# Kernel optimization log

Hardware: AMD Instinct MI355X
Metric: run time of the kernel (lower is better)

Reference implementation:

```python
import jax, jax.numpy as jnp
import numpy as np

N_NODES = 100000
N_EDGES = 1600000
F_IN = 128
HIDDEN = [128, 128]
F_OUT = 64


def _glorot(key, shape):
    fan_in, fan_out = shape[1], shape[0]
    lim = jnp.sqrt(6.0 / (fan_in + fan_out))
    return jax.random.uniform(key, shape, jnp.float32, -lim, lim)


def setup_inputs() -> dict:
    key = jax.random.key(0)
    ks = jax.random.split(key, 12)
    x = jax.random.normal(ks[0], (N_NODES, F_IN), jnp.float32)
    edge_index = jax.random.randint(ks[1], (2, N_EDGES), 0, N_NODES, jnp.int64)
    dims = [F_IN] + HIDDEN + [F_OUT]  # [128, 128, 128, 64]
    inp = {"x": x, "edge_index": edge_index}
    for i in range(3):
        din, dout = dims[i], dims[i + 1]
        inp[f"Wl{i}"] = _glorot(ks[2 + 3 * i], (dout, din))  # neighbor lin (lin_l)
        inp[f"Wr{i}"] = _glorot(ks[3 + 3 * i], (dout, din))  # root lin (lin_r)
        inp[f"b{i}"] = jnp.zeros((dout,), jnp.float32)
    return inp


def sage_conv(x, src, dst, Wl, Wr, b):
    # PyG SAGEConv, aggr='mean': out = lin_l(mean_{j in N(i)} x_j) + lin_r(x_i) + bias
    msg = x[src]  # [E, Fin] gather from source nodes
    agg = jax.ops.segment_sum(msg, dst, num_segments=N_NODES)  # [N, Fin]
    deg = jax.ops.segment_sum(jnp.ones((src.shape[0],), x.dtype), dst,
                              num_segments=N_NODES)  # [N]
    mean = agg / jnp.maximum(deg, 1.0)[:, None]
    return mean @ Wl.T + x @ Wr.T + b


def reference(x, edge_index, Wl0, Wr0, b0, Wl1, Wr1, b1, Wl2, Wr2, b2):
    src, dst = edge_index[0], edge_index[1]
    h = jax.nn.relu(sage_conv(x, src, dst, Wl0, Wr0, b0))
    h = jax.nn.relu(sage_conv(h, src, dst, Wl1, Wr1, b1))
    out = sage_conv(h, src, dst, Wl2, Wr2, b2)  # final_conv: no relu
    return out
```

## Files before the change

### kernel.cpp

```cpp
#include <hip/hip_runtime.h>

#define NF 128
#define CHUNK 4096

typedef __attribute__((ext_vector_type(8))) short bf16x8;
typedef __attribute__((ext_vector_type(4))) float f32x4;
typedef __attribute__((ext_vector_type(2))) float f32x2;

__device__ __forceinline__ unsigned short f2b(float f) {
    unsigned int u = __float_as_uint(f);
    unsigned int r = (u + 0x7fffu + ((u >> 16) & 1u)) >> 16;
    return (unsigned short)r;
}

__device__ __forceinline__ void gld_lds16(const void* g, const void* l) {
    __builtin_amdgcn_global_load_lds(
        (const __attribute__((address_space(1))) unsigned int*)(unsigned long long)g,
        (__attribute__((address_space(3))) unsigned int*)(unsigned int)(unsigned long long)l,
        16, 0, 0);
}


__global__ __launch_bounds__(256) void hist_kernel(const int* __restrict__ dst,
                                                   int* __restrict__ hist,
                                                   int E, int NB) {
    __shared__ int h[512];
    const int blk = blockIdx.x;
    for (int i = threadIdx.x; i < NB; i += 256) h[i] = 0;
    __syncthreads();
    const int e0 = blk * CHUNK;
    for (int i = threadIdx.x; i < CHUNK; i += 256) {
        int e = e0 + i;
        if (e < E) atomicAdd(&h[dst[e] >> 8], 1);
    }
    __syncthreads();
    for (int i = threadIdx.x; i < NB; i += 256) hist[blk * NB + i] = h[i];
}

__global__ __launch_bounds__(256) void sb_sum(const int* __restrict__ hist,
                                              int* __restrict__ bsum,
                                              int T, int NB, int NBLK) {
    int i = blockIdx.x * 256 + threadIdx.x;
    int v = 0;
    if (i < T) {
        int b = i / NBLK, blk = i - b * NBLK;
        v = hist[blk * NB + b];
    }
#pragma unroll
    for (int d = 32; d; d >>= 1) v += __shfl_down(v, d, 64);
    __shared__ int wsum[4];
    if ((threadIdx.x & 63) == 0) wsum[threadIdx.x >> 6] = v;
    __syncthreads();
    if (threadIdx.x == 0) bsum[blockIdx.x] = wsum[0] + wsum[1] + wsum[2] + wsum[3];
}

__global__ __launch_bounds__(1024) void sb_scan(const int* __restrict__ bsum,
                                                int* __restrict__ bpre, int NS) {
    __shared__ int s[1024];
    int t = threadIdx.x;
    int v = (t < NS) ? bsum[t] : 0;
    s[t] = v;
    __syncthreads();
    for (int d = 1; d < 1024; d <<= 1) {
        int u = (t >= d) ? s[t - d] : 0;
        __syncthreads();
        s[t] += u;
        __syncthreads();
    }
    if (t < NS) bpre[t] = s[t] - v;
}

__global__ __launch_bounds__(256) void sb_apply(const int* __restrict__ hist,
                                                const int* __restrict__ bpre,
                                                int* __restrict__ base,
                                                int T, int NB, int NBLK) {
    __shared__ int s[256];
    int i = blockIdx.x * 256 + threadIdx.x;
    int t = threadIdx.x;
    int v = 0;
    if (i < T) {
        int b = i / NBLK, blk = i - b * NBLK;
        v = hist[blk * NB + b];
    }
    s[t] = v;
    __syncthreads();
    for (int d = 1; d < 256; d <<= 1) {
        int u = (t >= d) ? s[t - d] : 0;
        __syncthreads();
        s[t] += u;
        __syncthreads();
    }
    if (i < T) base[i] = bpre[blockIdx.x] + s[t] - v;
}

__global__ __launch_bounds__(512) void bstart_kernel(const int* __restrict__ base,
                                                     int* __restrict__ bstart,
                                                     int NB, int NBLK, int E) {
    int i = threadIdx.x;
    if (i < NB) bstart[i] = base[i * NBLK];
    if (i == NB) bstart[i] = E;
}

__global__ __launch_bounds__(256) void scat_kernel(const int* __restrict__ src,
                                                   const int* __restrict__ dst,
                                                   const int* __restrict__ base,
                                                   unsigned int* __restrict__ recs,
                                                   int E, int NB, int NBLK) {
    __shared__ int cur[512];
    const int blk = blockIdx.x;
    for (int b = threadIdx.x; b < NB; b += 256) cur[b] = base[b * NBLK + blk];
    __syncthreads();
    const int e0 = blk * CHUNK;
    for (int i = threadIdx.x; i < CHUNK; i += 256) {
        int e = e0 + i;
        if (e >= E) continue;
        int d = dst[e];
        int b = d >> 8;
        int pos = atomicAdd(&cur[b], 1);
        recs[pos] = (unsigned int)src[e] | ((unsigned int)(d & 255) << 24);
    }
}

__global__ __launch_bounds__(256) void csr_kernel(const unsigned int* __restrict__ recs,
                                                  const int* __restrict__ bstart,
                                                  int* __restrict__ offs,
                                                  float* __restrict__ rdeg,
                                                  int* __restrict__ csr,
                                                  int N, int E) {
    __shared__ int cnt[256];
    __shared__ int sc[256];
    __shared__ int cur[256];
    const int b = blockIdx.x;
    const int t = threadIdx.x;
    const int s0 = bstart[b], s1 = bstart[b + 1];
    cnt[t] = 0;
    __syncthreads();
    for (int i = s0 + t; i < s1; i += 256) atomicAdd(&cnt[recs[i] >> 24], 1);
    __syncthreads();
    int v = cnt[t];
    sc[t] = v;
    __syncthreads();
    for (int d = 1; d < 256; d <<= 1) {
        int u = (t >= d) ? sc[t - d] : 0;
        __syncthreads();
        sc[t] += u;
        __syncthreads();
    }
    int excl = sc[t] - v;
    int node = b * 256 + t;
    if (node < N) {
        offs[node] = s0 + excl;
        rdeg[node] = 1.0f / (float)(v > 1 ? v : 1);
        if (node == N - 1) offs[N] = E;
    }
    cur[t] = s0 + excl;
    __syncthreads();
    for (int i = s0 + t; i < s1; i += 256) {
        unsigned int r = recs[i];
        int pos = atomicAdd(&cur[r >> 24], 1);
        csr[pos] = (int)(r & 0xFFFFFFu);
    }
}


__global__ void cvt_kernel(const float* __restrict__ x, unsigned short* __restrict__ xb, int n4) {
    int i = blockIdx.x * 256 + threadIdx.x;
    if (i >= n4) return;
    float4 v = *(const float4*)&x[(size_t)i * 4];
    uint2 o;
    o.x = (unsigned int)f2b(v.x) | ((unsigned int)f2b(v.y) << 16);
    o.y = (unsigned int)f2b(v.z) | ((unsigned int)f2b(v.w) << 16);
    *(uint2*)&xb[(size_t)i * 4] = o;
}

__global__ void wcat_kernel(const float* __restrict__ Wl, const float* __restrict__ Wr,
                            unsigned short* __restrict__ Wc, int total ) {
    int i = blockIdx.x * 256 + threadIdx.x;
    if (i >= total) return;
    int f = i >> 7, k = i & 127;
    Wc[f * 256 + k] = f2b(Wl[i]);
    Wc[f * 256 + 128 + k] = f2b(Wr[i]);
}

__global__ void wstack_kernel(const float* __restrict__ Wl, const float* __restrict__ Wr,
                              const float* __restrict__ b2,
                              unsigned short* __restrict__ Wst, float* __restrict__ bst,
                              int total ) {
    int i = blockIdx.x * 256 + threadIdx.x;
    if (i >= total) return;
    int f = i >> 7, k = i & 127;
    Wst[f * 128 + k] = f2b(Wl[i]);
    Wst[(f + 64) * 128 + k] = f2b(Wr[i]);
    if (k == 0) {
        bst[f] = 0.f;
        bst[f + 64] = b2[f];
    }
}


__global__ __launch_bounds__(256) void agg_kernel(
        const unsigned short* __restrict__ h, const int* __restrict__ offs,
        const int* __restrict__ csr, const float* __restrict__ rdeg,
        unsigned short* __restrict__ meanout, int N) {
    const int node = blockIdx.x * 4 + (threadIdx.x >> 6);
    const int lane = threadIdx.x & 63;
    if (node >= N) return;
    const int s0 = offs[node], s1 = offs[node + 1];
    const char* hb = (const char*)h;
    f32x2 acc = {0.f, 0.f};
    for (int base = s0; base < s1; base += 64) {
        const int cnt = min(64, s1 - base);
        const int boff = csr[base + min(lane, cnt - 1)] << 8;
        for (int j = 0; j < cnt; j += 16) {
            if (j + 16 <= cnt) {
                int o[16];
#pragma unroll
                for (int k = 0; k < 16; ++k) o[k] = __shfl(boff, j + k, 64);
                unsigned int v[16];
#pragma unroll
                for (int k = 0; k < 16; ++k)
                    v[k] = *(const unsigned int*)(hb + o[k] + lane * 4);
#pragma unroll
                for (int k = 0; k < 16; ++k)
                    acc += (f32x2){__uint_as_float(v[k] << 16),
                                   __uint_as_float(v[k] & 0xffff0000u)};
            } else {
                int o[16];
#pragma unroll
                for (int k = 0; k < 16; ++k) o[k] = __shfl(boff, min(j + k, cnt - 1), 64);
                unsigned int v[16];
#pragma unroll
                for (int k = 0; k < 16; ++k)
                    v[k] = *(const unsigned int*)(hb + o[k] + lane * 4);
#pragma unroll
                for (int k = 0; k < 16; ++k)
                    if (j + k < cnt)
                        acc += (f32x2){__uint_as_float(v[k] << 16),
                                       __uint_as_float(v[k] & 0xffff0000u)};
            }
        }
    }
    float r = rdeg[node];
    unsigned int o = (unsigned int)f2b(acc.x * r) | ((unsigned int)f2b(acc.y * r) << 16);
    *(unsigned int*)&meanout[(size_t)node * NF + lane * 2] = o;
}


__global__ __launch_bounds__(256) void agg2_kernel(
        const unsigned short* __restrict__ z, const int* __restrict__ offs,
        const int* __restrict__ csr, const float* __restrict__ rdeg,
        float* __restrict__ out, int N) {
    const int node = blockIdx.x * 4 + (threadIdx.x >> 6);
    const int lane = threadIdx.x & 63;
    if (node >= N) return;
    const int hlf = lane >> 5;
    const int fl  = lane & 31;
    const int s0 = offs[node], s1 = offs[node + 1];
    const char* zb = (const char*)z;
    f32x2 acc = {0.f, 0.f};
    for (int base = s0; base < s1; base += 64) {
        const int cnt = min(64, s1 - base);
        const int boff = csr[base + min(lane, cnt - 1)] << 8;
        for (int j = 0; j < cnt; j += 16) {
            if (j + 16 <= cnt) {
                int o[8];
#pragma unroll
                for (int k = 0; k < 8; ++k) o[k] = __shfl(boff, j + 2 * k + hlf, 64);
                unsigned int v[8];
#pragma unroll
                for (int k = 0; k < 8; ++k)
                    v[k] = *(const unsigned int*)(zb + o[k] + fl * 4);
#pragma unroll
                for (int k = 0; k < 8; ++k)
                    acc += (f32x2){__uint_as_float(v[k] << 16),
                                   __uint_as_float(v[k] & 0xffff0000u)};
            } else {
                int o[8];
#pragma unroll
                for (int k = 0; k < 8; ++k)
                    o[k] = __shfl(boff, min(j + 2 * k + hlf, cnt - 1), 64);
                unsigned int v[8];
#pragma unroll
                for (int k = 0; k < 8; ++k)
                    v[k] = *(const unsigned int*)(zb + o[k] + fl * 4);
#pragma unroll
                for (int k = 0; k < 8; ++k)
                    if (j + 2 * k + hlf < cnt)
                        acc += (f32x2){__uint_as_float(v[k] << 16),
                                       __uint_as_float(v[k] & 0xffff0000u)};
            }
        }
    }
    acc.x += __shfl_xor(acc.x, 32, 64);
    acc.y += __shfl_xor(acc.y, 32, 64);
    if (hlf == 0) {
        float r = rdeg[node];
        unsigned int vr = *(const unsigned int*)(zb + (size_t)node * 256 + 128 + fl * 4);
        float2 o;
        o.x = acc.x * r + __uint_as_float(vr << 16);
        o.y = acc.y * r + __uint_as_float(vr & 0xffff0000u);
        *(float2*)&out[(size_t)node * 64 + fl * 2] = o;
    }
}


template <int FOUT, bool RELU>
__global__ __launch_bounds__(256) void gemm_kernel(
        const unsigned short* __restrict__ Abuf,
        const unsigned short* __restrict__ Hbuf,
        const unsigned short* __restrict__ Wcat,
        const float* __restrict__ bias,
        unsigned short* __restrict__ outb,
        int N) {
    __shared__ unsigned short As[128 * 256];
    __shared__ unsigned short Ws[FOUT * 256];

    const int tid = threadIdx.x, wid = tid >> 6, lane = tid & 63;
    const int m0 = blockIdx.x * 128;
    char* Ac = (char*)As;
    char* Wc = (char*)Ws;
    const char* Ab = (const char*)Abuf;
    const char* Hb = (const char*)Hbuf;
    const char* Wb = (const char*)Wcat;

#pragma unroll
    for (int i = 0; i < 16; ++i) {
        int off = wid * 16384 + i * 1024 + lane * 16;
        int row = off >> 9, c = off & 511;
        int c2 = c ^ ((row & 7) << 4);
        const char* srcp = (c2 < 256) ? (Ab + (size_t)(m0 + row) * 256 + c2)
                                      : (Hb + (size_t)(m0 + row) * 256 + (c2 - 256));
        gld_lds16(srcp, Ac + wid * 16384 + i * 1024);
    }
#pragma unroll
    for (int i = 0; i < FOUT / 8; ++i) {
        int off = wid * (FOUT * 128) + i * 1024 + lane * 16;
        int row = off >> 9, c = off & 511;
        int c2 = c ^ ((row & 7) << 4);
        gld_lds16(Wb + (size_t)row * 512 + c2, Wc + wid * (FOUT * 128) + i * 1024);
    }
    asm volatile("s_waitcnt vmcnt(0)" ::: "memory");
    __syncthreads();

    constexpr int MI = (FOUT == 128) ? 4 : 2;
    constexpr int NI = 4;
    const int lm = lane & 15, ko = lane >> 4;
    const int wmBase = (FOUT == 128) ? (wid >> 1) * 64 : wid * 32;
    const int wnBase = (FOUT == 128) ? (wid & 1) * 64 : 0;

    f32x4 acc[MI][NI];
#pragma unroll
    for (int i = 0; i < MI; ++i)
#pragma unroll
        for (int j = 0; j < NI; ++j)
            acc[i][j] = (f32x4){0.f, 0.f, 0.f, 0.f};

#pragma unroll
    for (int ks = 0; ks < 8; ++ks) {
        const int kb = ks * 64 + ko * 16;
        bf16x8 a[MI], b[NI];
#pragma unroll
        for (int i = 0; i < MI; ++i) {
            int row = wmBase + i * 16 + lm;
            a[i] = *(const bf16x8*)(Ac + row * 512 + (kb ^ ((row & 7) << 4)));
        }
#pragma unroll
        for (int j = 0; j < NI; ++j) {
            int row = wnBase + j * 16 + lm;
            b[j] = *(const bf16x8*)(Wc + row * 512 + (kb ^ ((row & 7) << 4)));
        }
#pragma unroll
        for (int i = 0; i < MI; ++i)
#pragma unroll
            for (int j = 0; j < NI; ++j)
                acc[i][j] = __builtin_amdgcn_mfma_f32_16x16x32_bf16(b[j], a[i], acc[i][j], 0, 0, 0);
    }

#pragma unroll
    for (int i = 0; i < MI; ++i) {
        const int node = m0 + wmBase + i * 16 + lm;
        if (node < N) {
#pragma unroll
            for (int j = 0; j < NI; ++j) {
                const int col0 = wnBase + j * 16 + ko * 4;
                const float4 bv = *(const float4*)&bias[col0];
                float v0 = acc[i][j][0] + bv.x;
                float v1 = acc[i][j][1] + bv.y;
                float v2 = acc[i][j][2] + bv.z;
                float v3 = acc[i][j][3] + bv.w;
                if (RELU) {
                    v0 = fmaxf(v0, 0.f); v1 = fmaxf(v1, 0.f);
                    v2 = fmaxf(v2, 0.f); v3 = fmaxf(v3, 0.f);
                }
                uint2 o;
                o.x = (unsigned int)f2b(v0) | ((unsigned int)f2b(v1) << 16);
                o.y = (unsigned int)f2b(v2) | ((unsigned int)f2b(v3) << 16);
                *(uint2*)&outb[(size_t)node * FOUT + col0] = o;
            }
        }
    }
}


__global__ __launch_bounds__(256) void gemmz_kernel(
        const unsigned short* __restrict__ A,
        const unsigned short* __restrict__ W,
        const float* __restrict__ bias,
        unsigned short* __restrict__ outb,
        int N) {
    __shared__ unsigned short As[128 * 128];
    __shared__ unsigned short Ws[128 * 128];

    const int tid = threadIdx.x, wid = tid >> 6, lane = tid & 63;
    const int m0 = blockIdx.x * 128;
    char* Ac = (char*)As;
    char* Wc = (char*)Ws;
    const char* Ab = (const char*)A;
    const char* Wb = (const char*)W;

#pragma unroll
    for (int i = 0; i < 8; ++i) {
        int off = wid * 8192 + i * 1024 + lane * 16;
        int row = off >> 8, c = off & 255;
        int c2 = c ^ ((row & 7) << 4);
        gld_lds16(Ab + (size_t)(m0 + row) * 256 + c2, Ac + wid * 8192 + i * 1024);
    }
#pragma unroll
    for (int i = 0; i < 8; ++i) {
        int off = wid * 8192 + i * 1024 + lane * 16;
        int row = off >> 8, c = off & 255;
        int c2 = c ^ ((row & 7) << 4);
        gld_lds16(Wb + (size_t)row * 256 + c2, Wc + wid * 8192 + i * 1024);
    }
    asm volatile("s_waitcnt vmcnt(0)" ::: "memory");
    __syncthreads();

    const int lm = lane & 15, ko = lane >> 4;
    const int wmBase = (wid >> 1) * 64;
    const int wnBase = (wid & 1) * 64;

    f32x4 acc[4][4];
#pragma unroll
    for (int i = 0; i < 4; ++i)
#pragma unroll
        for (int j = 0; j < 4; ++j)
            acc[i][j] = (f32x4){0.f, 0.f, 0.f, 0.f};

#pragma unroll
    for (int ks = 0; ks < 4; ++ks) {
        const int kb = ks * 64 + ko * 16;
        bf16x8 a[4], b[4];
#pragma unroll
        for (int i = 0; i < 4; ++i) {
            int row = wmBase + i * 16 + lm;
            a[i] = *(const bf16x8*)(Ac + row * 256 + (kb ^ ((row & 7) << 4)));
        }
#pragma unroll
        for (int j = 0; j < 4; ++j) {
            int row = wnBase + j * 16 + lm;
            b[j] = *(const bf16x8*)(Wc + row * 256 + (kb ^ ((row & 7) << 4)));
        }
#pragma unroll
        for (int i = 0; i < 4; ++i)
#pragma unroll
            for (int j = 0; j < 4; ++j)
                acc[i][j] = __builtin_amdgcn_mfma_f32_16x16x32_bf16(b[j], a[i], acc[i][j], 0, 0, 0);
    }

#pragma unroll
    for (int i = 0; i < 4; ++i) {
        const int node = m0 + wmBase + i * 16 + lm;
        if (node < N) {
#pragma unroll
            for (int j = 0; j < 4; ++j) {
                const int col0 = wnBase + j * 16 + ko * 4;
                const float4 bv = *(const float4*)&bias[col0];
                uint2 o;
                o.x = (unsigned int)f2b(acc[i][j][0] + bv.x) |
                      ((unsigned int)f2b(acc[i][j][1] + bv.y) << 16);
                o.y = (unsigned int)f2b(acc[i][j][2] + bv.z) |
                      ((unsigned int)f2b(acc[i][j][3] + bv.w) << 16);
                *(uint2*)&outb[(size_t)node * 128 + col0] = o;
            }
        }
    }
}


extern "C" void kernel_launch(void* const* d_in, const int* in_sizes, int n_in,
                              void* d_out, int out_size, void* d_ws, size_t ws_size,
                              hipStream_t stream) {
    const float* x   = (const float*)d_in[0];
    const int*   ei  = (const int*)d_in[1];
    const float* Wl0 = (const float*)d_in[2];
    const float* Wr0 = (const float*)d_in[3];
    const float* b0  = (const float*)d_in[4];
    const float* Wl1 = (const float*)d_in[5];
    const float* Wr1 = (const float*)d_in[6];
    const float* b1  = (const float*)d_in[7];
    const float* Wl2 = (const float*)d_in[8];
    const float* Wr2 = (const float*)d_in[9];
    const float* b2  = (const float*)d_in[10];
    float* out = (float*)d_out;

    const int N = in_sizes[0] / NF;
    const int E = in_sizes[1] / 2;
    const int* srcv = ei;
    const int* dstv = ei + E;

    const int NB   = (N + 255) >> 8;
    const int NBLK = (E + CHUNK - 1) / CHUNK;
    const int T    = NB * NBLK;
    const int NS   = (T + 255) / 256;

    char* w = (char*)d_ws;
    auto alloc = [&](size_t bytes) {
        void* p = (void*)w;
        w += (bytes + 255) & ~(size_t)255;
        return p;
    };
    unsigned short* xb   = (unsigned short*)alloc((size_t)N * NF * 2);
    unsigned short* h1b  = (unsigned short*)alloc((size_t)N * NF * 2);
    unsigned short* h2b  = (unsigned short*)alloc((size_t)N * NF * 2);
    unsigned short* mb   = (unsigned short*)alloc((size_t)N * NF * 2);
    unsigned short* z2b  = (unsigned short*)alloc((size_t)N * NF * 2);
    unsigned short* Wc0  = (unsigned short*)alloc((size_t)128 * 256 * 2);
    unsigned short* Wc1  = (unsigned short*)alloc((size_t)128 * 256 * 2);
    unsigned short* Wst2 = (unsigned short*)alloc((size_t)128 * 128 * 2);
    float*          bst2 = (float*)alloc((size_t)128 * 4);
    int*   offs   = (int*)alloc((size_t)(N + 1) * 4);
    int*   csr    = (int*)alloc((size_t)E * 4);
    float* rdeg   = (float*)alloc((size_t)N * 4);
    unsigned int* recs = (unsigned int*)alloc((size_t)E * 4);
    int*   hist   = (int*)alloc((size_t)T * 4);
    int*   base   = (int*)alloc((size_t)T * 4);
    int*   bstart = (int*)alloc((size_t)(NB + 1) * 4);
    int*   sb1    = (int*)alloc((size_t)1024 * 4);
    int*   sb2    = (int*)alloc((size_t)1024 * 4);

    const int n4 = N * NF / 4;
    cvt_kernel<<<(n4 + 255) / 256, 256, 0, stream>>>(x, xb, n4);
    wcat_kernel<<<(128 * 128 + 255) / 256, 256, 0, stream>>>(Wl0, Wr0, Wc0, 128 * 128);
    wcat_kernel<<<(128 * 128 + 255) / 256, 256, 0, stream>>>(Wl1, Wr1, Wc1, 128 * 128);
    wstack_kernel<<<(64 * 128 + 255) / 256, 256, 0, stream>>>(Wl2, Wr2, b2, Wst2, bst2, 64 * 128);

    hist_kernel<<<NBLK, 256, 0, stream>>>(dstv, hist, E, NB);
    sb_sum<<<NS, 256, 0, stream>>>(hist, sb1, T, NB, NBLK);
    sb_scan<<<1, 1024, 0, stream>>>(sb1, sb2, NS);
    sb_apply<<<NS, 256, 0, stream>>>(hist, sb2, base, T, NB, NBLK);
    bstart_kernel<<<1, 512, 0, stream>>>(base, bstart, NB, NBLK, E);
    scat_kernel<<<NBLK, 256, 0, stream>>>(srcv, dstv, base, recs, E, NB, NBLK);
    csr_kernel<<<NB, 256, 0, stream>>>(recs, bstart, offs, rdeg, csr, N, E);

    const int ab = (N + 3) / 4;
    const int gb = (N + 127) / 128;

    agg_kernel<<<ab, 256, 0, stream>>>(xb, offs, csr, rdeg, mb, N);
    gemm_kernel<128, true><<<gb, 256, 0, stream>>>(mb, xb, Wc0, b0, h1b, N);

    agg_kernel<<<ab, 256, 0, stream>>>(h1b, offs, csr, rdeg, mb, N);
    gemm_kernel<128, true><<<gb, 256, 0, stream>>>(mb, h1b, Wc1, b1, h2b, N);

    gemmz_kernel<<<gb, 256, 0, stream>>>(h2b, Wst2, bst2, z2b, N);
    agg2_kernel<<<ab, 256, 0, stream>>>(z2b, offs, csr, rdeg, out, N);
}
```

Before: 298.6 us.

## Merge prep kernels, fold bstart into scan, read GEMM weights from global

Merges the x conversion, the three weight packing kernels and the destination histogram into a single launch whose work is chosen by block-index ranges. The bstart computation moves into sb_apply, dropping another launch. Both GEMM kernels stop staging the weight tile in LDS and read B fragments directly from global memory, relying on caching; this frees LDS but adds global load latency inside the MFMA loop. The aggregation kernels precompute lane byte offsets and add restrict qualifiers.

```diff
diff --git a/kernel.cpp b/kernel.cpp
--- a/kernel.cpp
+++ b/kernel.cpp
@@ -21,21 +21,58 @@
 }
 
 
-__global__ __launch_bounds__(256) void hist_kernel(const int* __restrict__ dst,
-                                                   int* __restrict__ hist,
-                                                   int E, int NB) {
-    __shared__ int h[512];
+__global__ __launch_bounds__(256) void prep_kernel(
+        const float* __restrict__ x, unsigned short* __restrict__ xb, int n4,
+        const float* __restrict__ Wl0, const float* __restrict__ Wr0, unsigned short* __restrict__ Wc0,
+        const float* __restrict__ Wl1, const float* __restrict__ Wr1, unsigned short* __restrict__ Wc1,
+        const float* __restrict__ Wl2, const float* __restrict__ Wr2, const float* __restrict__ b2,
+        unsigned short* __restrict__ Wst, float* __restrict__ bst,
+        const int* __restrict__ dst, int* __restrict__ hist, int E, int NB,
+        int bCvt, int bW0, int bW1, int bWs) {
+    __shared__ int hsh[512];
     const int blk = blockIdx.x;
-    for (int i = threadIdx.x; i < NB; i += 256) h[i] = 0;
-    __syncthreads();
-    const int e0 = blk * CHUNK;
-    for (int i = threadIdx.x; i < CHUNK; i += 256) {
-        int e = e0 + i;
-        if (e < E) atomicAdd(&h[dst[e] >> 8], 1);
-    }
-    __syncthreads();
-    for (int i = threadIdx.x; i < NB; i += 256) hist[blk * NB + i] = h[i];
-}
+    const int tid = threadIdx.x;
+    if (blk < bCvt) {
+        int i = blk * 256 + tid;
+        if (i < n4) {
+            float4 v = *(const float4*)&x[(size_t)i * 4];
+            uint2 o;
+            o.x = (unsigned int)f2b(v.x) | ((unsigned int)f2b(v.y) << 16);
+            o.y = (unsigned int)f2b(v.z) | ((unsigned int)f2b(v.w) << 16);
+            *(uint2*)&xb[(size_t)i * 4] = o;
+        }
+    } else if (blk < bW1) {
+        const bool first = blk < bW0;
+        int i = (blk - (first ? bCvt : bW0)) * 256 + tid;
+        const float* Wl = first ? Wl0 : Wl1;
+        const float* Wr = first ? Wr0 : Wr1;
+        unsigned short* Wc = first ? Wc0 : Wc1;
+        int f = i >> 7, k = i & 127;
+        Wc[f * 256 + k] = f2b(Wl[i]);
+        Wc[f * 256 + 128 + k] = f2b(Wr[i]);
+    } else if (blk < bWs) {
+        int i = (blk - bW1) * 256 + tid;
+        int f = i >> 7, k = i & 127;
+        Wst[f * 128 + k] = f2b(Wl2[i]);
+        Wst[(f + 64) * 128 + k] = f2b(Wr2[i]);
+        if (k == 0) {
+            bst[f] = 0.f;
+            bst[f + 64] = b2[f];
+        }
+    } else {
+        const int hb = blk - bWs;
+        for (int i = tid; i < NB; i += 256) hsh[i] = 0;
+        __syncthreads();
+        const int e0 = hb * CHUNK;
+        for (int i = tid; i < CHUNK; i += 256) {
+            int e = e0 + i;
+            if (e < E) atomicAdd(&hsh[dst[e] >> 8], 1);
+        }
+        __syncthreads();
+        for (int i = tid; i < NB; i += 256) hist[hb * NB + i] = hsh[i];
+    }
+}
+
 
 __global__ __launch_bounds__(256) void sb_sum(const int* __restrict__ hist,
                                               int* __restrict__ bsum,
@@ -73,13 +110,16 @@
 __global__ __launch_bounds__(256) void sb_apply(const int* __restrict__ hist,
                                                 const int* __restrict__ bpre,
                                                 int* __restrict__ base,
-                                                int T, int NB, int NBLK) {
+                                                int* __restrict__ bstart,
+                                                int T, int NB, int NBLK, int E) {
     __shared__ int s[256];
     int i = blockIdx.x * 256 + threadIdx.x;
     int t = threadIdx.x;
     int v = 0;
+    int b = 0, blk = 0;
     if (i < T) {
-        int b = i / NBLK, blk = i - b * NBLK;
+        b = i / NBLK;
+        blk = i - b * NBLK;
         v = hist[blk * NB + b];
     }
     s[t] = v;
@@ -90,15 +130,12 @@
         s[t] += u;
         __syncthreads();
     }
-    if (i < T) base[i] = bpre[blockIdx.x] + s[t] - v;
-}
-
-__global__ __launch_bounds__(512) void bstart_kernel(const int* __restrict__ base,
-                                                     int* __restrict__ bstart,
-                                                     int NB, int NBLK, int E) {
-    int i = threadIdx.x;
-    if (i < NB) bstart[i] = base[i * NBLK];
-    if (i == NB) bstart[i] = E;
+    if (i < T) {
+        int val = bpre[blockIdx.x] + s[t] - v;
+        base[i] = val;
+        if (blk == 0) bstart[b] = val;
+        if (i == 0) bstart[NB] = E;
+    }
 }
 
 __global__ __launch_bounds__(256) void scat_kernel(const int* __restrict__ src,
@@ -163,41 +200,6 @@
 }
 
 
-__global__ void cvt_kernel(const float* __restrict__ x, unsigned short* __restrict__ xb, int n4) {
-    int i = blockIdx.x * 256 + threadIdx.x;
-    if (i >= n4) return;
-    float4 v = *(const float4*)&x[(size_t)i * 4];
-    uint2 o;
-    o.x = (unsigned int)f2b(v.x) | ((unsigned int)f2b(v.y) << 16);
-    o.y = (unsigned int)f2b(v.z) | ((unsigned int)f2b(v.w) << 16);
-    *(uint2*)&xb[(size_t)i * 4] = o;
-}
-
-__global__ void wcat_kernel(const float* __restrict__ Wl, const float* __restrict__ Wr,
-                            unsigned short* __restrict__ Wc, int total ) {
-    int i = blockIdx.x * 256 + threadIdx.x;
-    if (i >= total) return;
-    int f = i >> 7, k = i & 127;
-    Wc[f * 256 + k] = f2b(Wl[i]);
-    Wc[f * 256 + 128 + k] = f2b(Wr[i]);
-}
-
-__global__ void wstack_kernel(const float* __restrict__ Wl, const float* __restrict__ Wr,
-                              const float* __restrict__ b2,
-                              unsigned short* __restrict__ Wst, float* __restrict__ bst,
-                              int total ) {
-    int i = blockIdx.x * 256 + threadIdx.x;
-    if (i >= total) return;
-    int f = i >> 7, k = i & 127;
-    Wst[f * 128 + k] = f2b(Wl[i]);
-    Wst[(f + 64) * 128 + k] = f2b(Wr[i]);
-    if (k == 0) {
-        bst[f] = 0.f;
-        bst[f + 64] = b2[f];
-    }
-}
-
-
 __global__ __launch_bounds__(256) void agg_kernel(
         const unsigned short* __restrict__ h, const int* __restrict__ offs,
         const int* __restrict__ csr, const float* __restrict__ rdeg,
@@ -206,32 +208,35 @@
     const int lane = threadIdx.x & 63;
     if (node >= N) return;
     const int s0 = offs[node], s1 = offs[node + 1];
-    const char* hb = (const char*)h;
+    const char* __restrict__ hb = (const char*)h;
+    const unsigned lane4 = (unsigned)lane * 4u;
     f32x2 acc = {0.f, 0.f};
     for (int base = s0; base < s1; base += 64) {
         const int cnt = min(64, s1 - base);
         const int boff = csr[base + min(lane, cnt - 1)] << 8;
         for (int j = 0; j < cnt; j += 16) {
             if (j + 16 <= cnt) {
-                int o[16];
-#pragma unroll
-                for (int k = 0; k < 16; ++k) o[k] = __shfl(boff, j + k, 64);
+                unsigned o[16];
+#pragma unroll
+                for (int k = 0; k < 16; ++k)
+                    o[k] = (unsigned)__shfl(boff, j + k, 64) + lane4;
                 unsigned int v[16];
 #pragma unroll
                 for (int k = 0; k < 16; ++k)
-                    v[k] = *(const unsigned int*)(hb + o[k] + lane * 4);
+                    v[k] = *(const unsigned int*)(hb + o[k]);
 #pragma unroll
                 for (int k = 0; k < 16; ++k)
                     acc += (f32x2){__uint_as_float(v[k] << 16),
                                    __uint_as_float(v[k] & 0xffff0000u)};
             } else {
-                int o[16];
-#pragma unroll
-                for (int k = 0; k < 16; ++k) o[k] = __shfl(boff, min(j + k, cnt - 1), 64);
+                unsigned o[16];
+#pragma unroll
+                for (int k = 0; k < 16; ++k)
+                    o[k] = (unsigned)__shfl(boff, min(j + k, cnt - 1), 64) + lane4;
                 unsigned int v[16];
 #pragma unroll
                 for (int k = 0; k < 16; ++k)
-                    v[k] = *(const unsigned int*)(hb + o[k] + lane * 4);
+                    v[k] = *(const unsigned int*)(hb + o[k]);
 #pragma unroll
                 for (int k = 0; k < 16; ++k)
                     if (j + k < cnt)
@@ -256,33 +261,35 @@
     const int hlf = lane >> 5;
     const int fl  = lane & 31;
     const int s0 = offs[node], s1 = offs[node + 1];
-    const char* zb = (const char*)z;
+    const char* __restrict__ zb = (const char*)z;
+    const unsigned fl4 = (unsigned)fl * 4u;
     f32x2 acc = {0.f, 0.f};
     for (int base = s0; base < s1; base += 64) {
         const int cnt = min(64, s1 - base);
         const int boff = csr[base + min(lane, cnt - 1)] << 8;
         for (int j = 0; j < cnt; j += 16) {
             if (j + 16 <= cnt) {
-                int o[8];
-#pragma unroll
-                for (int k = 0; k < 8; ++k) o[k] = __shfl(boff, j + 2 * k + hlf, 64);
+                unsigned o[8];
+#pragma unroll
+                for (int k = 0; k < 8; ++k)
+                    o[k] = (unsigned)__shfl(boff, j + 2 * k + hlf, 64) + fl4;
                 unsigned int v[8];
 #pragma unroll
                 for (int k = 0; k < 8; ++k)
-                    v[k] = *(const unsigned int*)(zb + o[k] + fl * 4);
+                    v[k] = *(const unsigned int*)(zb + o[k]);
 #pragma unroll
                 for (int k = 0; k < 8; ++k)
                     acc += (f32x2){__uint_as_float(v[k] << 16),
                                    __uint_as_float(v[k] & 0xffff0000u)};
             } else {
-                int o[8];
+                unsigned o[8];
 #pragma unroll
                 for (int k = 0; k < 8; ++k)
-                    o[k] = __shfl(boff, min(j + 2 * k + hlf, cnt - 1), 64);
+                    o[k] = (unsigned)__shfl(boff, min(j + 2 * k + hlf, cnt - 1), 64) + fl4;
                 unsigned int v[8];
 #pragma unroll
                 for (int k = 0; k < 8; ++k)
-                    v[k] = *(const unsigned int*)(zb + o[k] + fl * 4);
+                    v[k] = *(const unsigned int*)(zb + o[k]);
 #pragma unroll
                 for (int k = 0; k < 8; ++k)
                     if (j + 2 * k + hlf < cnt)
@@ -313,12 +320,10 @@
         unsigned short* __restrict__ outb,
         int N) {
     __shared__ unsigned short As[128 * 256];
-    __shared__ unsigned short Ws[FOUT * 256];
 
     const int tid = threadIdx.x, wid = tid >> 6, lane = tid & 63;
     const int m0 = blockIdx.x * 128;
     char* Ac = (char*)As;
-    char* Wc = (char*)Ws;
     const char* Ab = (const char*)Abuf;
     const char* Hb = (const char*)Hbuf;
     const char* Wb = (const char*)Wcat;
@@ -332,13 +337,6 @@
                                       : (Hb + (size_t)(m0 + row) * 256 + (c2 - 256));
         gld_lds16(srcp, Ac + wid * 16384 + i * 1024);
     }
-#pragma unroll
-    for (int i = 0; i < FOUT / 8; ++i) {
-        int off = wid * (FOUT * 128) + i * 1024 + lane * 16;
-        int row = off >> 9, c = off & 511;
-        int c2 = c ^ ((row & 7) << 4);
-        gld_lds16(Wb + (size_t)row * 512 + c2, Wc + wid * (FOUT * 128) + i * 1024);
-    }
     asm volatile("s_waitcnt vmcnt(0)" ::: "memory");
     __syncthreads();
 
@@ -360,14 +358,14 @@
         const int kb = ks * 64 + ko * 16;
         bf16x8 a[MI], b[NI];
 #pragma unroll
+        for (int j = 0; j < NI; ++j) {
+            int row = wnBase + j * 16 + lm;
+            b[j] = *(const bf16x8*)(Wb + row * 512 + kb);
+        }
+#pragma unroll
         for (int i = 0; i < MI; ++i) {
             int row = wmBase + i * 16 + lm;
             a[i] = *(const bf16x8*)(Ac + row * 512 + (kb ^ ((row & 7) << 4)));
-        }
-#pragma unroll
-        for (int j = 0; j < NI; ++j) {
-            int row = wnBase + j * 16 + lm;
-            b[j] = *(const bf16x8*)(Wc + row * 512 + (kb ^ ((row & 7) << 4)));
         }
 #pragma unroll
         for (int i = 0; i < MI; ++i)
@@ -409,12 +407,10 @@
         unsigned short* __restrict__ outb,
         int N) {
     __shared__ unsigned short As[128 * 128];
-    __shared__ unsigned short Ws[128 * 128];
 
     const int tid = threadIdx.x, wid = tid >> 6, lane = tid & 63;
     const int m0 = blockIdx.x * 128;
     char* Ac = (char*)As;
-    char* Wc = (char*)Ws;
     const char* Ab = (const char*)A;
     const char* Wb = (const char*)W;
 
@@ -425,13 +421,6 @@
         int c2 = c ^ ((row & 7) << 4);
         gld_lds16(Ab + (size_t)(m0 + row) * 256 + c2, Ac + wid * 8192 + i * 1024);
     }
-#pragma unroll
-    for (int i = 0; i < 8; ++i) {
-        int off = wid * 8192 + i * 1024 + lane * 16;
-        int row = off >> 8, c = off & 255;
-        int c2 = c ^ ((row & 7) << 4);
-        gld_lds16(Wb + (size_t)row * 256 + c2, Wc + wid * 8192 + i * 1024);
-    }
     asm volatile("s_waitcnt vmcnt(0)" ::: "memory");
     __syncthreads();
 
@@ -451,14 +440,14 @@
         const int kb = ks * 64 + ko * 16;
         bf16x8 a[4], b[4];
 #pragma unroll
+        for (int j = 0; j < 4; ++j) {
+            int row = wnBase + j * 16 + lm;
+            b[j] = *(const bf16x8*)(Wb + row * 256 + kb);
+        }
+#pragma unroll
         for (int i = 0; i < 4; ++i) {
             int row = wmBase + i * 16 + lm;
             a[i] = *(const bf16x8*)(Ac + row * 256 + (kb ^ ((row & 7) << 4)));
-        }
-#pragma unroll
-        for (int j = 0; j < 4; ++j) {
-            int row = wnBase + j * 16 + lm;
-            b[j] = *(const bf16x8*)(Wc + row * 256 + (kb ^ ((row & 7) << 4)));
         }
 #pragma unroll
         for (int i = 0; i < 4; ++i)
@@ -539,16 +528,20 @@
     int*   sb2    = (int*)alloc((size_t)1024 * 4);
 
     const int n4 = N * NF / 4;
-    cvt_kernel<<<(n4 + 255) / 256, 256, 0, stream>>>(x, xb, n4);
-    wcat_kernel<<<(128 * 128 + 255) / 256, 256, 0, stream>>>(Wl0, Wr0, Wc0, 128 * 128);
-    wcat_kernel<<<(128 * 128 + 255) / 256, 256, 0, stream>>>(Wl1, Wr1, Wc1, 128 * 128);
-    wstack_kernel<<<(64 * 128 + 255) / 256, 256, 0, stream>>>(Wl2, Wr2, b2, Wst2, bst2, 64 * 128);
-
-    hist_kernel<<<NBLK, 256, 0, stream>>>(dstv, hist, E, NB);
+    const int bCvt = (n4 + 255) / 256;
+    const int bW0  = bCvt + 64;
+    const int bW1  = bW0 + 64;
+    const int bWs  = bW1 + 32;
+    const int bTot = bWs + NBLK;
+
+    prep_kernel<<<bTot, 256, 0, stream>>>(x, xb, n4,
+                                          Wl0, Wr0, Wc0, Wl1, Wr1, Wc1,
+                                          Wl2, Wr2, b2, Wst2, bst2,
+                                          dstv, hist, E, NB,
+                                          bCvt, bW0, bW1, bWs);
     sb_sum<<<NS, 256, 0, stream>>>(hist, sb1, T, NB, NBLK);
     sb_scan<<<1, 1024, 0, stream>>>(sb1, sb2, NS);
-    sb_apply<<<NS, 256, 0, stream>>>(hist, sb2, base, T, NB, NBLK);
-    bstart_kernel<<<1, 512, 0, stream>>>(base, bstart, NB, NBLK, E);
+    sb_apply<<<NS, 256, 0, stream>>>(hist, sb2, base, bstart, T, NB, NBLK, E);
     scat_kernel<<<NBLK, 256, 0, stream>>>(srcv, dstv, base, recs, E, NB, NBLK);
     csr_kernel<<<NB, 256, 0, stream>>>(recs, bstart, offs, rdeg, csr, N, E);
 
```

New measurement: 302.5 us. About the same (+1.3%).
